# Kernel optimization log

Measured on AMD Instinct MI355X. Metric: run time of the kernel, lower is better.

Reference implementation:

```python
import jax, jax.numpy as jnp
import numpy as np

B, N, F_IN, F_OUT = 8, 2048, 256, 256
NEG_SLOPE = 0.2
EPS = 1e-7


def setup_inputs() -> dict:
    key = jax.random.key(0)
    k1, k2, k3, k4, k5 = jax.random.split(key, 5)
    x = jax.random.normal(k1, (B, N, F_IN), dtype=jnp.float32)
    # A is a 0/1 adjacency mask used as float in the module
    A = jax.random.bernoulli(k2, 0.5, (B, N, N)).astype(jnp.float32)
    # W: xavier_normal_ init, shape [in_features, out_features]
    W = jax.random.normal(k3, (F_IN, F_OUT), dtype=jnp.float32) * np.sqrt(2.0 / (F_IN + F_OUT))
    # attention_mechanism: Linear(2*F_OUT, 1) -> weight vector [2*F_OUT], scalar bias
    bound = 1.0 / np.sqrt(2 * F_OUT)
    a_w = jax.random.uniform(k4, (2 * F_OUT,), dtype=jnp.float32, minval=-bound, maxval=bound)
    a_b = jax.random.uniform(k5, (), dtype=jnp.float32, minval=-bound, maxval=bound)
    return {"A": A, "x": x, "W": W, "a_w": a_w, "a_b": a_b}


def reference(A, x, W, a_w, a_b):
    # Wh = x @ W : [B, N, F_OUT]
    Wh = jnp.einsum('bnf,fo->bno', x, W)
    # Linear([Wh_i ; Wh_j]) == Wh_i @ a_w[:F] + Wh_j @ a_w[F:] + b  (no O(N^2 F) concat)
    s_src = Wh @ a_w[:F_OUT]   # [B, N] contribution of row index i
    s_dst = Wh @ a_w[F_OUT:]   # [B, N] contribution of col index j
    e = s_src[:, :, None] + s_dst[:, None, :] + a_b  # [B, N, N]
    e = jnp.where(e > 0, e, NEG_SLOPE * e)           # leaky_relu(0.2)
    # masked softmax over dim=1 (as in the original module)
    exps = jnp.exp(e) * A
    sums = jnp.sum(exps, axis=1, keepdims=True) + EPS
    attn = exps / sums                                # [B, N, N]
    return jnp.einsum('bij,bjo->bio', attn, Wh)       # [B, N, F_OUT]
```

## Files before the change

kernel.cpp:

```cpp
#include <hip/hip_runtime.h>
#include <hip/hip_bf16.h>

#define NN 2048
#define BB 8
#define FD 256
#define NEG_SLOPE 0.2f
#define EPSV 1e-7f
#define PSTR 36

typedef __bf16 bf16x8 __attribute__((ext_vector_type(8)));
typedef __bf16 bf16x4 __attribute__((ext_vector_type(4)));
typedef float f32x4 __attribute__((ext_vector_type(4)));

__device__ __forceinline__ void gload16(const __bf16* g, __bf16* l) {
    __builtin_amdgcn_global_load_lds((const __attribute__((address_space(1))) unsigned int*)g,
                                     (__attribute__((address_space(3))) unsigned int*)l,
                                     16, 0, 0);
}

__global__ __launch_bounds__(256) void k1_prep(const float* __restrict__ W,
                                               __bf16* __restrict__ WT) {
    int idx = blockIdx.x * 256 + threadIdx.x;
    int o = idx >> 8, f = idx & 255;
    WT[idx] = (__bf16)W[f * FD + o];
}

__global__ __launch_bounds__(256) void k2_whgemm(const float* __restrict__ x,
                                                 const __bf16* __restrict__ WT,
                                                 const float* __restrict__ a_w,
                                                 float* __restrict__ Wh,
                                                 float* __restrict__ s_src,
                                                 float* __restrict__ s_dst) {
    const int wave = threadIdx.x >> 6;
    const int lane = threadIdx.x & 63;
    const int row0 = blockIdx.x * 32 + (wave >> 1) * 16;
    const int ohalf = (wave & 1) * 128;
    const int m = lane & 15;
    const int quad = lane >> 4;
    const int row = row0 + m;
    const float* xrow = x + (size_t)row * FD + quad * 8;

    f32x4 acc[8];
#pragma unroll
    for (int n = 0; n < 8; ++n) acc[n] = (f32x4){0.f, 0.f, 0.f, 0.f};

    for (int k0 = 0; k0 < FD; k0 += 32) {
        float4 xa = *(const float4*)(xrow + k0);
        float4 xb = *(const float4*)(xrow + k0 + 4);
        bf16x8 af;
        af[0] = (__bf16)xa.x; af[1] = (__bf16)xa.y; af[2] = (__bf16)xa.z; af[3] = (__bf16)xa.w;
        af[4] = (__bf16)xb.x; af[5] = (__bf16)xb.y; af[6] = (__bf16)xb.z; af[7] = (__bf16)xb.w;
#pragma unroll
        for (int n = 0; n < 8; ++n) {
            int o = ohalf + n * 16 + m;
            bf16x8 bf = *(const bf16x8*)(WT + o * FD + k0 + quad * 8);
            acc[n] = __builtin_amdgcn_mfma_f32_16x16x32_bf16(af, bf, acc[n], 0, 0, 0);
        }
    }
#pragma unroll
    for (int n = 0; n < 8; ++n) {
        int o = ohalf + n * 16 + m;
#pragma unroll
        for (int r = 0; r < 4; ++r) {
            Wh[(size_t)(row0 + quad * 4 + r) * FD + o] = acc[n][r];
        }
    }

    float psrc[4] = {0.f, 0.f, 0.f, 0.f};
    float pdst[4] = {0.f, 0.f, 0.f, 0.f};
#pragma unroll
    for (int n = 0; n < 8; ++n) {
        int o = ohalf + n * 16 + m;
        float awS = a_w[o], awD = a_w[FD + o];
#pragma unroll
        for (int r = 0; r < 4; ++r) {
            psrc[r] += acc[n][r] * awS;
            pdst[r] += acc[n][r] * awD;
        }
    }
#pragma unroll
    for (int off = 1; off <= 8; off <<= 1) {
#pragma unroll
        for (int r = 0; r < 4; ++r) {
            psrc[r] += __shfl_xor(psrc[r], off, 64);
            pdst[r] += __shfl_xor(pdst[r], off, 64);
        }
    }
    __shared__ float sS[2][2][16], sD[2][2][16];
    if (m == 0) {
        int rp = wave >> 1, oh = wave & 1;
#pragma unroll
        for (int r = 0; r < 4; ++r) {
            sS[rp][oh][quad * 4 + r] = psrc[r];
            sD[rp][oh][quad * 4 + r] = pdst[r];
        }
    }
    __syncthreads();
    if (threadIdx.x < 32) {
        int rp = threadIdx.x >> 4, idx = threadIdx.x & 15;
        int orow = blockIdx.x * 32 + rp * 16 + idx;
        s_src[orow] = sS[rp][0][idx] + sS[rp][1][idx];
        s_dst[orow] = sD[rp][0][idx] + sD[rp][1][idx];
    }
}

__global__ __launch_bounds__(256) void k4_den(const float* __restrict__ A,
                                              const float* __restrict__ s_src,
                                              const float* __restrict__ s_dst,
                                              const float* __restrict__ a_bp,
                                              float* __restrict__ den_part,
                                              unsigned char* __restrict__ Apack) {
    const int blk = blockIdx.x;
    const int b = blk & 7;
    const int jhalf = (blk >> 3) & 1;
    const int isp = blk >> 4;
    const int i0 = isp * 32;
    const int j = jhalf * 1024 + threadIdx.x * 4;
    __shared__ float ss[32];
    if (threadIdx.x < 32) ss[threadIdx.x] = s_src[b * NN + i0 + threadIdx.x] + a_bp[0];
    __syncthreads();
    float4 sd = *(const float4*)(s_dst + b * NN + j);
    float ax = 0.f, ay = 0.f, az = 0.f, aw = 0.f;
    const float* Ap = A + ((size_t)b * NN + i0) * NN + j;
    unsigned char* Pk = Apack + ((size_t)(b * NN + i0)) * 512 + jhalf * 256 + threadIdx.x;
#pragma unroll 8
    for (int i = 0; i < 32; ++i) {
        float4 a = *(const float4*)(Ap + (size_t)i * NN);
        float si = ss[i];
        float e0 = si + sd.x; e0 = e0 > 0.f ? e0 : NEG_SLOPE * e0;
        float e1 = si + sd.y; e1 = e1 > 0.f ? e1 : NEG_SLOPE * e1;
        float e2 = si + sd.z; e2 = e2 > 0.f ? e2 : NEG_SLOPE * e2;
        float e3 = si + sd.w; e3 = e3 > 0.f ? e3 : NEG_SLOPE * e3;
        ax += a.x * __expf(e0);
        ay += a.y * __expf(e1);
        az += a.z * __expf(e2);
        aw += a.w * __expf(e3);
        unsigned nib = (a.x > 0.5f ? 1u : 0u) | (a.y > 0.5f ? 2u : 0u) |
                       (a.z > 0.5f ? 4u : 0u) | (a.w > 0.5f ? 8u : 0u);
        Pk[(size_t)i * 512] = (unsigned char)nib;
    }
    float4 r = (float4){ax, ay, az, aw};
    *(float4*)(den_part + (size_t)isp * (BB * NN) + b * NN + j) = r;
}

__global__ __launch_bounds__(256) void k5_wht(const float* __restrict__ Wh,
                                              const float* __restrict__ den_part,
                                              __bf16* __restrict__ WhT) {
    const int b = blockIdx.z;
    const int j0 = blockIdx.x * 64;
    const int o0 = blockIdx.y * 64;
    __shared__ float tile[64][65];
    __shared__ float invd[64];
    if (threadIdx.x < 64) {
        float s = 0.f;
        const float* dp = den_part + b * NN + j0 + threadIdx.x;
#pragma unroll 8
        for (int sI = 0; sI < 64; ++sI) s += dp[(size_t)sI * (BB * NN)];
        invd[threadIdx.x] = 1.f / (s + EPSV);
    }
    __syncthreads();
    int jr = threadIdx.x >> 4, oc = (threadIdx.x & 15) * 4;
#pragma unroll
    for (int p = 0; p < 4; ++p) {
        int jj = jr + p * 16;
        float4 v = *(const float4*)(Wh + (size_t)(b * NN + j0 + jj) * FD + o0 + oc);
        float s = invd[jj];
        tile[jj][oc + 0] = v.x * s;
        tile[jj][oc + 1] = v.y * s;
        tile[jj][oc + 2] = v.z * s;
        tile[jj][oc + 3] = v.w * s;
    }
    __syncthreads();
    int ow = threadIdx.x >> 4, jc = (threadIdx.x & 15) * 4;
#pragma unroll
    for (int p = 0; p < 4; ++p) {
        int o = ow + p * 16;
        bf16x4 wv;
        wv[0] = (__bf16)tile[jc + 0][o];
        wv[1] = (__bf16)tile[jc + 1][o];
        wv[2] = (__bf16)tile[jc + 2][o];
        wv[3] = (__bf16)tile[jc + 3][o];
        *(bf16x4*)(WhT + (size_t)(b * FD + o0 + o) * NN + j0 + jc) = wv;
    }
}

__global__ __launch_bounds__(256) void k6_out(const unsigned char* __restrict__ Apack,
                                              const __bf16* __restrict__ WhT,
                                              const float* __restrict__ s_src,
                                              const float* __restrict__ s_dst,
                                              const float* __restrict__ a_bp,
                                              float* __restrict__ out) {
    __shared__ __bf16 Pt[2][32 * PSTR];
    __shared__ __bf16 Bt[2][128 * 32];
    const int blk = blockIdx.x;
    const int b = blk & 7;
    const int r_ = blk >> 3;
    const int itile = r_ & 63;
    const int oh = r_ >> 6;
    const int i0 = itile * 32;
    const int o0 = oh * 128;
    const int t = threadIdx.x;
    const int w = t >> 6, lane = t & 63;
    const int m = lane & 15, quad = lane >> 4;
    const int wrow = w >> 1, wcol = w & 1;

    const int prow = t >> 3, pjq = t & 7;
    const float ssr = s_src[b * NN + i0 + prow] + a_bp[0];
    const unsigned char* Apb = Apack + ((size_t)(b * NN + i0 + prow)) * 512 + pjq;
    const float* sdbase = s_dst + b * NN + pjq * 4;
    __bf16* Pw = &Pt[0][0] + prow * PSTR + pjq * 4;
    const int pstep = 32 * PSTR;

    const __bf16* gB0 = WhT + ((size_t)(b * FD + o0 + w * 16 + (lane >> 2))) * NN + (lane & 3) * 8;
    const __bf16* gB1 = gB0 + (size_t)64 * NN;
    __bf16* lB0 = &Bt[0][0] + (w * 16) * 32;
    __bf16* lB1 = &Bt[0][0] + (w * 16 + 64) * 32;
    const int lstepB = 128 * 32;

    unsigned ab = Apb[0];
    float4 q0 = *(const float4*)(sdbase);
    gload16(gB0, lB0);
    gload16(gB1, lB1);

#define BUILD_P(dstbuf)                                                          \
    {                                                                            \
        bf16x4 pv; float e;                                                      \
        e = ssr + q0.x; e = e > 0.f ? e : NEG_SLOPE * e;                         \
        pv[0] = (__bf16)((ab & 1u) ? __expf(e) : 0.f);                           \
        e = ssr + q0.y; e = e > 0.f ? e : NEG_SLOPE * e;                         \
        pv[1] = (__bf16)((ab & 2u) ? __expf(e) : 0.f);                           \
        e = ssr + q0.z; e = e > 0.f ? e : NEG_SLOPE * e;                         \
        pv[2] = (__bf16)((ab & 4u) ? __expf(e) : 0.f);                           \
        e = ssr + q0.w; e = e > 0.f ? e : NEG_SLOPE * e;                         \
        pv[3] = (__bf16)((ab & 8u) ? __expf(e) : 0.f);                           \
        *(bf16x4*)(Pw + (dstbuf) * pstep) = pv;                                  \
    }

    BUILD_P(0)

    f32x4 acc[4];
#pragma unroll
    for (int n = 0; n < 4; ++n) acc[n] = (f32x4){0.f, 0.f, 0.f, 0.f};

    const __bf16* Pr = &Pt[0][0] + (wrow * 16 + m) * PSTR + quad * 8;
    const __bf16* Br = &Bt[0][0] + (wcol * 64 + m) * 32 + quad * 8;

    for (int kk = 0; kk < 64; ++kk) {
        __syncthreads();
        const int cur = kk & 1, nb = cur ^ 1;
        if (kk < 63) {
            gload16(gB0 + (kk + 1) * 32, lB0 + nb * lstepB);
            gload16(gB1 + (kk + 1) * 32, lB1 + nb * lstepB);
            ab = Apb[(kk + 1) * 8];
            q0 = *(const float4*)(sdbase + (kk + 1) * 32);
        }
        const __bf16* Pk = Pr + cur * pstep;
        const __bf16* Bk = Br + cur * lstepB;
        bf16x8 af = *(const bf16x8*)(Pk);
#pragma unroll
        for (int n = 0; n < 4; ++n) {
            bf16x8 bfr = *(const bf16x8*)(Bk + n * 16 * 32);
            acc[n] = __builtin_amdgcn_mfma_f32_16x16x32_bf16(af, bfr, acc[n], 0, 0, 0);
        }
        if (kk < 63) BUILD_P(nb)
    }

#pragma unroll
    for (int n = 0; n < 4; ++n) {
        int o = o0 + wcol * 64 + n * 16 + m;
#pragma unroll
        for (int rr = 0; rr < 4; ++rr) {
            int orow = i0 + wrow * 16 + quad * 4 + rr;
            out[((size_t)b * NN + orow) * FD + o] = acc[n][rr];
        }
    }
#undef BUILD_P
}

extern "C" void kernel_launch(void* const* d_in, const int* in_sizes, int n_in,
                              void* d_out, int out_size, void* d_ws, size_t ws_size,
                              hipStream_t stream) {
    const float* A   = (const float*)d_in[0];
    const float* x   = (const float*)d_in[1];
    const float* W   = (const float*)d_in[2];
    const float* a_w = (const float*)d_in[3];
    const float* a_b = (const float*)d_in[4];
    float* out = (float*)d_out;

    char* ws = (char*)d_ws;
    __bf16* WT      = (__bf16*)ws;
    float*  Wh      = (float*)(ws + 131072);
    __bf16* WhT     = (__bf16*)(ws + 16908288);
    float*  s_src   = (float*)(ws + 25296896);
    float*  s_dst   = (float*)(ws + 25362432);
    float*  den_part= (float*)(ws + 25427968);
    unsigned char* Apack = (unsigned char*)(ws + 29622272);

    k1_prep<<<256, 256, 0, stream>>>(W, WT);
    k2_whgemm<<<512, 256, 0, stream>>>(x, WT, a_w, Wh, s_src, s_dst);
    k4_den<<<1024, 256, 0, stream>>>(A, s_src, s_dst, a_b, den_part, Apack);
    k5_wht<<<dim3(32, 4, 8), 256, 0, stream>>>(Wh, den_part, WhT);
    k6_out<<<1024, 256, 0, stream>>>(Apack, WhT, s_src, s_dst, a_b, out);
}
```

Baseline: 303.8 us.

## Give each wave its own output-column slice and build P in registers without barriers

The output kernel is restructured so each block covers 16 rows and all 256 output columns, with each wave owning 64 columns and a private double-buffered LDS slice of WhT. The attention-weight fragment is computed directly in registers as the MFMA A operand, which removes the shared P tile and every __syncthreads in the main loop. In exchange, each wave recomputes the same exp values, so exp work per block doubles, and WhT traffic per output row rises. Correctness also relies on the compiler inserting the waits needed for the async LDS loads now that there is no barrier.

```diff
diff --git a/kernel.cpp b/kernel.cpp
--- a/kernel.cpp
+++ b/kernel.cpp
@@ -6,7 +6,6 @@
 #define FD 256
 #define NEG_SLOPE 0.2f
 #define EPSV 1e-7f
-#define PSTR 36
 
 typedef __bf16 bf16x8 __attribute__((ext_vector_type(8)));
 typedef __bf16 bf16x4 __attribute__((ext_vector_type(4)));
@@ -190,91 +189,73 @@
                                               const float* __restrict__ s_dst,
                                               const float* __restrict__ a_bp,
                                               float* __restrict__ out) {
-    __shared__ __bf16 Pt[2][32 * PSTR];
-    __shared__ __bf16 Bt[2][128 * 32];
+    __shared__ __bf16 Bt[4][2][64 * 32];
     const int blk = blockIdx.x;
     const int b = blk & 7;
-    const int r_ = blk >> 3;
-    const int itile = r_ & 63;
-    const int oh = r_ >> 6;
-    const int i0 = itile * 32;
-    const int o0 = oh * 128;
+    const int itile = blk >> 3;
+    const int i0 = itile * 16;
     const int t = threadIdx.x;
     const int w = t >> 6, lane = t & 63;
     const int m = lane & 15, quad = lane >> 4;
-    const int wrow = w >> 1, wcol = w & 1;
-
-    const int prow = t >> 3, pjq = t & 7;
-    const float ssr = s_src[b * NN + i0 + prow] + a_bp[0];
-    const unsigned char* Apb = Apack + ((size_t)(b * NN + i0 + prow)) * 512 + pjq;
-    const float* sdbase = s_dst + b * NN + pjq * 4;
-    __bf16* Pw = &Pt[0][0] + prow * PSTR + pjq * 4;
-    const int pstep = 32 * PSTR;
-
-    const __bf16* gB0 = WhT + ((size_t)(b * FD + o0 + w * 16 + (lane >> 2))) * NN + (lane & 3) * 8;
-    const __bf16* gB1 = gB0 + (size_t)64 * NN;
-    __bf16* lB0 = &Bt[0][0] + (w * 16) * 32;
-    __bf16* lB1 = &Bt[0][0] + (w * 16 + 64) * 32;
-    const int lstepB = 128 * 32;
-
-    unsigned ab = Apb[0];
-    float4 q0 = *(const float4*)(sdbase);
-    gload16(gB0, lB0);
-    gload16(gB1, lB1);
-
-#define BUILD_P(dstbuf)                                                          \
-    {                                                                            \
-        bf16x4 pv; float e;                                                      \
-        e = ssr + q0.x; e = e > 0.f ? e : NEG_SLOPE * e;                         \
-        pv[0] = (__bf16)((ab & 1u) ? __expf(e) : 0.f);                           \
-        e = ssr + q0.y; e = e > 0.f ? e : NEG_SLOPE * e;                         \
-        pv[1] = (__bf16)((ab & 2u) ? __expf(e) : 0.f);                           \
-        e = ssr + q0.z; e = e > 0.f ? e : NEG_SLOPE * e;                         \
-        pv[2] = (__bf16)((ab & 4u) ? __expf(e) : 0.f);                           \
-        e = ssr + q0.w; e = e > 0.f ? e : NEG_SLOPE * e;                         \
-        pv[3] = (__bf16)((ab & 8u) ? __expf(e) : 0.f);                           \
-        *(bf16x4*)(Pw + (dstbuf) * pstep) = pv;                                  \
-    }
-
-    BUILD_P(0)
+    const int o0 = w * 64;
+
+    const __bf16* gB = WhT + ((size_t)(b * FD + o0 + (lane >> 2))) * NN + (lane & 3) * 8;
+    __bf16* lB = &Bt[w][0][0];
+    const float ssr = s_src[b * NN + i0 + m] + a_bp[0];
+    const unsigned char* Apb = Apack + ((size_t)(b * NN + i0 + m)) * 512 + quad * 2;
+    const float* sdp = s_dst + b * NN + quad * 8;
+
+#pragma unroll
+    for (int c = 0; c < 4; ++c)
+        gload16(gB + (size_t)(c * 16) * NN, lB + c * 512);
 
     f32x4 acc[4];
 #pragma unroll
     for (int n = 0; n < 4; ++n) acc[n] = (f32x4){0.f, 0.f, 0.f, 0.f};
 
-    const __bf16* Pr = &Pt[0][0] + (wrow * 16 + m) * PSTR + quad * 8;
-    const __bf16* Br = &Bt[0][0] + (wcol * 64 + m) * 32 + quad * 8;
+    const __bf16* Br = lB + m * 32 + quad * 8;
 
     for (int kk = 0; kk < 64; ++kk) {
-        __syncthreads();
         const int cur = kk & 1, nb = cur ^ 1;
+        const __bf16* Bk = Br + cur * 2048;
+        bf16x8 bf0 = *(const bf16x8*)(Bk);
+        bf16x8 bf1 = *(const bf16x8*)(Bk + 16 * 32);
+        bf16x8 bf2 = *(const bf16x8*)(Bk + 32 * 32);
+        bf16x8 bf3 = *(const bf16x8*)(Bk + 48 * 32);
         if (kk < 63) {
-            gload16(gB0 + (kk + 1) * 32, lB0 + nb * lstepB);
-            gload16(gB1 + (kk + 1) * 32, lB1 + nb * lstepB);
-            ab = Apb[(kk + 1) * 8];
-            q0 = *(const float4*)(sdbase + (kk + 1) * 32);
-        }
-        const __bf16* Pk = Pr + cur * pstep;
-        const __bf16* Bk = Br + cur * lstepB;
-        bf16x8 af = *(const bf16x8*)(Pk);
-#pragma unroll
-        for (int n = 0; n < 4; ++n) {
-            bf16x8 bfr = *(const bf16x8*)(Bk + n * 16 * 32);
-            acc[n] = __builtin_amdgcn_mfma_f32_16x16x32_bf16(af, bfr, acc[n], 0, 0, 0);
-        }
-        if (kk < 63) BUILD_P(nb)
+#pragma unroll
+            for (int c = 0; c < 4; ++c)
+                gload16(gB + (size_t)(c * 16) * NN + (kk + 1) * 32, lB + nb * 2048 + c * 512);
+        }
+        unsigned short av = *(const unsigned short*)(Apb + kk * 8);
+        unsigned abits = (av & 0x0Fu) | ((av >> 4) & 0xF0u);
+        float4 q0 = *(const float4*)(sdp + kk * 32);
+        float4 q1 = *(const float4*)(sdp + kk * 32 + 4);
+        bf16x8 af;
+        float e;
+        e = ssr + q0.x; e = e > 0.f ? e : NEG_SLOPE * e; af[0] = (__bf16)((abits &   1u) ? __expf(e) : 0.f);
+        e = ssr + q0.y; e = e > 0.f ? e : NEG_SLOPE * e; af[1] = (__bf16)((abits &   2u) ? __expf(e) : 0.f);
+        e = ssr + q0.z; e = e > 0.f ? e : NEG_SLOPE * e; af[2] = (__bf16)((abits &   4u) ? __expf(e) : 0.f);
+        e = ssr + q0.w; e = e > 0.f ? e : NEG_SLOPE * e; af[3] = (__bf16)((abits &   8u) ? __expf(e) : 0.f);
+        e = ssr + q1.x; e = e > 0.f ? e : NEG_SLOPE * e; af[4] = (__bf16)((abits &  16u) ? __expf(e) : 0.f);
+        e = ssr + q1.y; e = e > 0.f ? e : NEG_SLOPE * e; af[5] = (__bf16)((abits &  32u) ? __expf(e) : 0.f);
+        e = ssr + q1.z; e = e > 0.f ? e : NEG_SLOPE * e; af[6] = (__bf16)((abits &  64u) ? __expf(e) : 0.f);
+        e = ssr + q1.w; e = e > 0.f ? e : NEG_SLOPE * e; af[7] = (__bf16)((abits & 128u) ? __expf(e) : 0.f);
+        acc[0] = __builtin_amdgcn_mfma_f32_16x16x32_bf16(af, bf0, acc[0], 0, 0, 0);
+        acc[1] = __builtin_amdgcn_mfma_f32_16x16x32_bf16(af, bf1, acc[1], 0, 0, 0);
+        acc[2] = __builtin_amdgcn_mfma_f32_16x16x32_bf16(af, bf2, acc[2], 0, 0, 0);
+        acc[3] = __builtin_amdgcn_mfma_f32_16x16x32_bf16(af, bf3, acc[3], 0, 0, 0);
     }
 
 #pragma unroll
     for (int n = 0; n < 4; ++n) {
-        int o = o0 + wcol * 64 + n * 16 + m;
+        int o = o0 + n * 16 + m;
 #pragma unroll
         for (int rr = 0; rr < 4; ++rr) {
-            int orow = i0 + wrow * 16 + quad * 4 + rr;
+            int orow = i0 + quad * 4 + rr;
             out[((size_t)b * NN + orow) * FD + o] = acc[n][rr];
         }
     }
-#undef BUILD_P
 }
 
 extern "C" void kernel_launch(void* const* d_in, const int* in_sizes, int n_in,
```

Result: slower. 328.4 us (+8.1%).
